# Performance work log

Measured on AMD Instinct MI355X. Metric: run time of the kernel, lower is better.

The kernel has to match this reference:

```python
import jax, jax.numpy as jnp
import numpy as np

N_NODES = 100000
N_EDGES = 1600000
IN_FEAT = 128
HID_FEAT = 128
OUT_FEAT = 128


def setup_inputs() -> dict:
    key = jax.random.key(0)
    k1, k2, k3, k4, k5 = jax.random.split(key, 5)
    x = jax.random.normal(k1, (N_NODES, IN_FEAT), dtype=jnp.float32)
    # Xavier-ish scale for weights
    W_in = jax.random.normal(k2, (2, IN_FEAT, HID_FEAT), dtype=jnp.float32) * (1.0 / np.sqrt(IN_FEAT))
    W_out = jax.random.normal(k3, (2, HID_FEAT, OUT_FEAT), dtype=jnp.float32) * (1.0 / np.sqrt(HID_FEAT))
    src = jax.random.randint(k4, (N_EDGES,), 0, N_NODES, dtype=jnp.int32)
    dst = jax.random.randint(k5, (N_EDGES,), 0, N_NODES, dtype=jnp.int32)
    return {"x": x, "W_in": W_in, "W_out": W_out, "src": src, "dst": dst}


def _mean_aggregate(h, src, dst, num_nodes):
    # copy_src('h','m') + fn.mean('m','neigh'): gather src feats, segment-mean by dst.
    msgs = h[src]                                             # [E, D]
    summed = jax.ops.segment_sum(msgs, dst, num_segments=num_nodes)   # [N, D]
    deg = jax.ops.segment_sum(jnp.ones((src.shape[0],), h.dtype), dst,
                              num_segments=num_nodes)         # [N]
    deg = jnp.maximum(deg, 1.0)                               # zero-in-degree -> 0 output
    return summed / deg[:, None]


def reference(x, W_in, W_out, src, dst):
    n = x.shape[0]
    # Layer 0 (i == 0): uses weight_in, ReLU activation (i != K-1)
    neigh = _mean_aggregate(x, src, dst, n)
    h = x @ W_in[0] + neigh @ W_in[1]
    h = jax.nn.relu(h)
    # Layer 1 (i == K-1): uses weight_out, no activation
    neigh = _mean_aggregate(h, src, dst, n)
    h = h @ W_out[0] + neigh @ W_out[1]
    return h
```

## Files before the change

### kernel.cpp

```cpp
#include <hip/hip_runtime.h>

#define NF 128
#define NBSHIFT 8
#define NBMAX 512
#define CHUNK 4096

typedef __attribute__((ext_vector_type(8))) short bf16x8;
typedef __attribute__((ext_vector_type(4))) float f32x4;
typedef __attribute__((ext_vector_type(2))) float f32x2;

__device__ __forceinline__ unsigned short f2bf(float f) {
    unsigned int u = __builtin_bit_cast(unsigned int, f);
    u = (u + 0x7fffu + ((u >> 16) & 1u)) >> 16;
    return (unsigned short)u;
}
__device__ __forceinline__ float bflo(unsigned int u) {
    return __builtin_bit_cast(float, u << 16);
}
__device__ __forceinline__ float bfhi(unsigned int u) {
    return __builtin_bit_cast(float, u & 0xffff0000u);
}
__device__ __forceinline__ unsigned char f2fp8(float v) {
    return (unsigned char)(__builtin_amdgcn_cvt_pk_fp8_f32(v, v, 0, false) & 0xff);
}

#define BH 256
#define BT 256
__global__ __launch_bounds__(256) void k_prep(const int* __restrict__ dst, int E, int NB,
                                              int* __restrict__ gbhist,
                                              const float* __restrict__ x,
                                              unsigned short* __restrict__ xb,
                                              unsigned char* __restrict__ xq,
                                              const float* __restrict__ Win,
                                              const float* __restrict__ Wout,
                                              unsigned short* __restrict__ BtIn,
                                              unsigned short* __restrict__ BtOut) {
    __shared__ int lh[NBMAX];
    const int bb = blockIdx.x;
    const int t = threadIdx.x;
    if (bb < BH) {
        for (int k = t; k < NBMAX; k += 256) lh[k] = 0;
        __syncthreads();
        for (int i = bb * 256 + t; i < E; i += BH * 256)
            atomicAdd(&lh[((unsigned)dst[i]) >> NBSHIFT], 1);
        __syncthreads();
        for (int k = t; k < NB; k += 256)
            if (lh[k]) atomicAdd(&gbhist[k], lh[k]);
    } else if (bb < BH + BT) {
        int b2 = bb - BH;
        const float* W = (b2 < 128) ? Win : Wout;
        unsigned short* Bt = (b2 < 128) ? BtIn : BtOut;
        int idx = (b2 & 127) * 256 + t;
        int c = idx >> 8;
        int k = idx & 255;
        int p = k >> 7, kk = k & 127;
        Bt[idx] = f2bf(W[((size_t)p * NF + kk) * NF + c]);
    } else {
        long long i = (long long)(bb - BH - BT) * 256 + t;
        const float4 a = *reinterpret_cast<const float4*>(x + i * 8);
        const float4 b = *reinterpret_cast<const float4*>(x + i * 8 + 4);
        union { unsigned short s[8]; uint4 u; } o;
        o.s[0] = f2bf(a.x); o.s[1] = f2bf(a.y); o.s[2] = f2bf(a.z); o.s[3] = f2bf(a.w);
        o.s[4] = f2bf(b.x); o.s[5] = f2bf(b.y); o.s[6] = f2bf(b.z); o.s[7] = f2bf(b.w);
        *reinterpret_cast<uint4*>(xb + i * 8) = o.u;
        int lo = __builtin_amdgcn_cvt_pk_fp8_f32(a.x, a.y, 0, false);
        lo = __builtin_amdgcn_cvt_pk_fp8_f32(a.z, a.w, lo, true);
        int hi = __builtin_amdgcn_cvt_pk_fp8_f32(b.x, b.y, 0, false);
        hi = __builtin_amdgcn_cvt_pk_fp8_f32(b.z, b.w, hi, true);
        uint2 oq; oq.x = (unsigned)lo; oq.y = (unsigned)hi;
        *reinterpret_cast<uint2*>(xq + i * 8) = oq;
    }
}


__global__ __launch_bounds__(256) void k_bscan(const int* __restrict__ gbhist,
                                               int* __restrict__ bbase, int* __restrict__ gcursor,
                                               int NB, int E, int* __restrict__ offsets, int n) {
    __shared__ int sA[NBMAX], sB[NBMAX];
    int t = threadIdx.x;
    for (int k = t; k < NBMAX; k += 256) sA[k] = (k < NB) ? gbhist[k] : 0;
    __syncthreads();
    int* pin = sA;
    int* pout = sB;
    for (int off = 1; off < NBMAX; off <<= 1) {
        for (int k = t; k < NBMAX; k += 256) pout[k] = pin[k] + (k >= off ? pin[k - off] : 0);
        __syncthreads();
        int* tmp = pin; pin = pout; pout = tmp;
    }
    for (int k = t; k < NB; k += 256) {
        int excl = pin[k] - gbhist[k];
        bbase[k] = excl;
        gcursor[k] = excl;
    }
    if (t == 0) {
        bbase[NB] = E;
        offsets[n] = E;
    }
}

__global__ __launch_bounds__(256) void k_bucket(const int* __restrict__ src,
                                                const int* __restrict__ dst,
                                                int* __restrict__ gcursor,
                                                unsigned* __restrict__ gpairs, int E) {
    __shared__ int lhist[NBMAX], lbase[NBMAX], lcur[NBMAX], gb[NBMAX];
    __shared__ int sA[NBMAX], sB[NBMAX];
    __shared__ unsigned stage[CHUNK];
    __shared__ unsigned short stage_b[CHUNK];
    const int t = threadIdx.x;
    const int c0 = blockIdx.x * CHUNK;
    const int cc = min(CHUNK, E - c0);

    for (int k = t; k < NBMAX; k += 256) lhist[k] = 0;
    __syncthreads();

    int ls[16], ld[16];
#pragma unroll
    for (int j = 0; j < 16; ++j) {
        int i = t + j * 256;
        ls[j] = 0; ld[j] = 0;
        if (i < cc) {
            ls[j] = src[c0 + i];
            ld[j] = dst[c0 + i];
            atomicAdd(&lhist[((unsigned)ld[j]) >> NBSHIFT], 1);
        }
    }
    __syncthreads();
    for (int k = t; k < NBMAX; k += 256) sA[k] = lhist[k];
    __syncthreads();
    int* pin = sA;
    int* pout = sB;
    for (int off = 1; off < NBMAX; off <<= 1) {
        for (int k = t; k < NBMAX; k += 256) pout[k] = pin[k] + (k >= off ? pin[k - off] : 0);
        __syncthreads();
        int* tmp = pin; pin = pout; pout = tmp;
    }
    for (int k = t; k < NBMAX; k += 256) {
        int excl = pin[k] - lhist[k];
        lbase[k] = excl;
        lcur[k] = excl;
        int cnt = lhist[k];
        if (cnt > 0) gb[k] = atomicAdd(&gcursor[k], cnt);
    }
    __syncthreads();
#pragma unroll
    for (int j = 0; j < 16; ++j) {
        int i = t + j * 256;
        if (i < cc) {
            int b = ((unsigned)ld[j]) >> NBSHIFT;
            int pos = atomicAdd(&lcur[b], 1);
            stage[pos] = (((unsigned)ld[j] & 255u) << 24) | (unsigned)ls[j];
            stage_b[pos] = (unsigned short)b;
        }
    }
    __syncthreads();
    for (int idx = t; idx < cc; idx += 256) {
        unsigned p = stage[idx];
        int b = stage_b[idx];
        gpairs[gb[b] + (idx - lbase[b])] = p;
    }
}

__global__ __launch_bounds__(256) void k_bsort(const unsigned* __restrict__ gpairs,
                                               const int* __restrict__ bbase,
                                               int* __restrict__ offsets,
                                               float* __restrict__ invdeg,
                                               int* __restrict__ esrc, int n) {
    __shared__ int lcnt[256], lcur[256], sA[256], sB[256];
    const int b = blockIdx.x;
    const int t = threadIdx.x;
    const int base = bbase[b];
    const int c = bbase[b + 1] - base;
    const int n0 = b << NBSHIFT;

    lcnt[t] = 0;
    __syncthreads();
    for (int i = t; i < c; i += 256) {
        int node = (int)(gpairs[base + i] >> 24);
        atomicAdd(&lcnt[node], 1);
    }
    __syncthreads();
    sA[t] = lcnt[t];
    __syncthreads();
    int* pin = sA;
    int* pout = sB;
    for (int off = 1; off < 256; off <<= 1) {
        pout[t] = pin[t] + (t >= off ? pin[t - off] : 0);
        __syncthreads();
        int* tmp = pin; pin = pout; pout = tmp;
    }
    int excl = pin[t] - lcnt[t];
    lcur[t] = excl;
    int node_g = n0 + t;
    if (node_g < n) {
        offsets[node_g] = base + excl;
        invdeg[node_g] = 1.0f / (float)max(lcnt[t], 1);
    }
    __syncthreads();
    for (int i = t; i < c; i += 256) {
        unsigned p = gpairs[base + i];
        int node = (int)(p >> 24);
        int pos = atomicAdd(&lcur[node], 1);
        esrc[base + pos] = (int)(p & 0x00ffffffu);
    }
}

__global__ __launch_bounds__(256) void k_agg_fp8(const unsigned char* __restrict__ feat,
                                                 const int* __restrict__ esrc,
                                                 const int* __restrict__ offsets,
                                                 const float* __restrict__ invdeg,
                                                 unsigned short* __restrict__ neigh, int n) {
    int wid0 = (int)(((long long)blockIdx.x * blockDim.x + threadIdx.x) >> 6);
    const int wid = __builtin_amdgcn_readfirstlane(wid0);
    if (wid >= n) return;
    const int lane = threadIdx.x & 63;
    const int g = lane >> 4;
    const int q = lane & 15;
    const unsigned qoff = (unsigned)q * 8u;
    const unsigned char* fb = feat;

    const int beg = offsets[wid];
    const int end = offsets[wid + 1];
    f32x2 c01 = {0.f, 0.f}, c23 = {0.f, 0.f}, c45 = {0.f, 0.f}, c67 = {0.f, 0.f};

    int i = beg;
    for (; i + 16 <= end; i += 16) {
        int e[16];
#pragma unroll
        for (int j = 0; j < 16; ++j) e[j] = esrc[i + j];
#pragma unroll
        for (int u = 0; u < 4; ++u) {
            int es = (g & 2) ? ((g & 1) ? e[u * 4 + 3] : e[u * 4 + 2])
                             : ((g & 1) ? e[u * 4 + 1] : e[u * 4 + 0]);
            uint2 v = *(const uint2*)(fb + (unsigned)es * 128u + qoff);
            c01 += __builtin_amdgcn_cvt_pk_f32_fp8((int)v.x, false);
            c23 += __builtin_amdgcn_cvt_pk_f32_fp8((int)v.x, true);
            c45 += __builtin_amdgcn_cvt_pk_f32_fp8((int)v.y, false);
            c67 += __builtin_amdgcn_cvt_pk_f32_fp8((int)v.y, true);
        }
    }
    for (; i + 4 <= end; i += 4) {
        int e0 = esrc[i + 0], e1 = esrc[i + 1], e2 = esrc[i + 2], e3 = esrc[i + 3];
        int es = (g & 2) ? ((g & 1) ? e3 : e2) : ((g & 1) ? e1 : e0);
        uint2 v = *(const uint2*)(fb + (unsigned)es * 128u + qoff);
        c01 += __builtin_amdgcn_cvt_pk_f32_fp8((int)v.x, false);
        c23 += __builtin_amdgcn_cvt_pk_f32_fp8((int)v.x, true);
        c45 += __builtin_amdgcn_cvt_pk_f32_fp8((int)v.y, false);
        c67 += __builtin_amdgcn_cvt_pk_f32_fp8((int)v.y, true);
    }
    if (i < end) {
        int r = end - i;
        if (g < r) {
            int es = esrc[i + g];
            uint2 v = *(const uint2*)(fb + (unsigned)es * 128u + qoff);
            c01 += __builtin_amdgcn_cvt_pk_f32_fp8((int)v.x, false);
            c23 += __builtin_amdgcn_cvt_pk_f32_fp8((int)v.x, true);
            c45 += __builtin_amdgcn_cvt_pk_f32_fp8((int)v.y, false);
            c67 += __builtin_amdgcn_cvt_pk_f32_fp8((int)v.y, true);
        }
    }
    float a0 = c01.x, a1 = c01.y, a2 = c23.x, a3 = c23.y;
    float a4 = c45.x, a5 = c45.y, a6 = c67.x, a7 = c67.y;
    a0 += __shfl_xor(a0, 16); a1 += __shfl_xor(a1, 16);
    a2 += __shfl_xor(a2, 16); a3 += __shfl_xor(a3, 16);
    a4 += __shfl_xor(a4, 16); a5 += __shfl_xor(a5, 16);
    a6 += __shfl_xor(a6, 16); a7 += __shfl_xor(a7, 16);
    a0 += __shfl_xor(a0, 32); a1 += __shfl_xor(a1, 32);
    a2 += __shfl_xor(a2, 32); a3 += __shfl_xor(a3, 32);
    a4 += __shfl_xor(a4, 32); a5 += __shfl_xor(a5, 32);
    a6 += __shfl_xor(a6, 32); a7 += __shfl_xor(a7, 32);

    const float sc = invdeg[wid];
    a0 *= sc; a1 *= sc; a2 *= sc; a3 *= sc;
    a4 *= sc; a5 *= sc; a6 *= sc; a7 *= sc;
    unsigned p0, p1, p2, p3;
    asm("v_cvt_pk_bf16_f32 %0, %1, %2" : "=v"(p0) : "v"(a0), "v"(a1));
    asm("v_cvt_pk_bf16_f32 %0, %1, %2" : "=v"(p1) : "v"(a2), "v"(a3));
    asm("v_cvt_pk_bf16_f32 %0, %1, %2" : "=v"(p2) : "v"(a4), "v"(a5));
    asm("v_cvt_pk_bf16_f32 %0, %1, %2" : "=v"(p3) : "v"(a6), "v"(a7));
    if (g == 0) {
        uint4 o; o.x = p0; o.y = p1; o.z = p2; o.w = p3;
        *(uint4*)((char*)neigh + (size_t)wid * 256 + (unsigned)q * 16u) = o;
    }
}

__global__ __launch_bounds__(256) void k_agg_bf16(const unsigned short* __restrict__ feat,
                                                  const int* __restrict__ esrc,
                                                  const int* __restrict__ offsets,
                                                  const float* __restrict__ invdeg,
                                                  unsigned short* __restrict__ neigh, int n) {
    int wid0 = (int)(((long long)blockIdx.x * blockDim.x + threadIdx.x) >> 6);
    const int wid = __builtin_amdgcn_readfirstlane(wid0);
    if (wid >= n) return;
    const int lane = threadIdx.x & 63;
    const int g = lane >> 4;
    const int q = lane & 15;
    const unsigned qoff = (unsigned)q * 16u;
    const char* fb = (const char*)feat;
    const int beg = offsets[wid];
    const int end = offsets[wid + 1];
    float a0 = 0.f, a1 = 0.f, a2 = 0.f, a3 = 0.f, a4 = 0.f, a5 = 0.f, a6 = 0.f, a7 = 0.f;
    int i = beg;
    for (; i + 4 <= end; i += 4) {
        int e0 = esrc[i + 0], e1 = esrc[i + 1], e2 = esrc[i + 2], e3 = esrc[i + 3];
        int es = (g & 2) ? ((g & 1) ? e3 : e2) : ((g & 1) ? e1 : e0);
        uint4 v = *(const uint4*)(fb + (unsigned)es * 256u + qoff);
        a0 += bflo(v.x); a1 += bfhi(v.x);
        a2 += bflo(v.y); a3 += bfhi(v.y);
        a4 += bflo(v.z); a5 += bfhi(v.z);
        a6 += bflo(v.w); a7 += bfhi(v.w);
    }
    if (i < end) {
        int r = end - i;
        if (g < r) {
            int es = esrc[i + g];
            uint4 v = *(const uint4*)(fb + (unsigned)es * 256u + qoff);
            a0 += bflo(v.x); a1 += bfhi(v.x);
            a2 += bflo(v.y); a3 += bfhi(v.y);
            a4 += bflo(v.z); a5 += bfhi(v.z);
            a6 += bflo(v.w); a7 += bfhi(v.w);
        }
    }
    a0 += __shfl_xor(a0, 16); a1 += __shfl_xor(a1, 16);
    a2 += __shfl_xor(a2, 16); a3 += __shfl_xor(a3, 16);
    a4 += __shfl_xor(a4, 16); a5 += __shfl_xor(a5, 16);
    a6 += __shfl_xor(a6, 16); a7 += __shfl_xor(a7, 16);
    a0 += __shfl_xor(a0, 32); a1 += __shfl_xor(a1, 32);
    a2 += __shfl_xor(a2, 32); a3 += __shfl_xor(a3, 32);
    a4 += __shfl_xor(a4, 32); a5 += __shfl_xor(a5, 32);
    a6 += __shfl_xor(a6, 32); a7 += __shfl_xor(a7, 32);
    const float sc = invdeg[wid];
    a0 *= sc; a1 *= sc; a2 *= sc; a3 *= sc;
    a4 *= sc; a5 *= sc; a6 *= sc; a7 *= sc;
    unsigned p0, p1, p2, p3;
    asm("v_cvt_pk_bf16_f32 %0, %1, %2" : "=v"(p0) : "v"(a0), "v"(a1));
    asm("v_cvt_pk_bf16_f32 %0, %1, %2" : "=v"(p1) : "v"(a2), "v"(a3));
    asm("v_cvt_pk_bf16_f32 %0, %1, %2" : "=v"(p2) : "v"(a4), "v"(a5));
    asm("v_cvt_pk_bf16_f32 %0, %1, %2" : "=v"(p3) : "v"(a6), "v"(a7));
    if (g == 0) {
        uint4 o; o.x = p0; o.y = p1; o.z = p2; o.w = p3;
        *(uint4*)((char*)neigh + (size_t)wid * 256 + qoff) = o;
    }
}

__global__ __launch_bounds__(256) void k_agg_f32(const float* __restrict__ feat,
                                                 const int* __restrict__ esrc,
                                                 const int* __restrict__ offsets,
                                                 const float* __restrict__ invdeg,
                                                 unsigned short* __restrict__ neigh, int n) {
    int wid0 = (int)(((long long)blockIdx.x * blockDim.x + threadIdx.x) >> 6);
    const int wid = __builtin_amdgcn_readfirstlane(wid0);
    if (wid >= n) return;
    int lane = threadIdx.x & 63;
    int beg = offsets[wid], end = offsets[wid + 1];
    float a0 = 0.f, a1 = 0.f;
    for (int i = beg; i < end; ++i) {
        int s0 = esrc[i];
        float2 v0 = *(const float2*)(feat + (size_t)s0 * NF + lane * 2);
        a0 += v0.x; a1 += v0.y;
    }
    float sc = invdeg[wid];
    unsigned pk;
    float ca = a0 * sc, cb = a1 * sc;
    asm("v_cvt_pk_bf16_f32 %0, %1, %2" : "=v"(pk) : "v"(ca), "v"(cb));
    *(unsigned*)(neigh + (size_t)wid * NF + lane * 2) = pk;
}

template <bool RELU, bool OUTBF16, bool WRITEQ>
__global__ __launch_bounds__(256) void k_gemm_lds(const unsigned short* __restrict__ A1,
                                                  const unsigned short* __restrict__ A2,
                                                  const unsigned short* __restrict__ Bt,
                                                  void* __restrict__ outv,
                                                  unsigned char* __restrict__ outq,
                                                  int nrows) {
    __shared__ __align__(16) unsigned char sm[32768];
    const int tid = threadIdx.x;
    const int w = tid >> 6;
    const int lane = tid & 63;
    const int l15 = lane & 15;
    const int lk = lane >> 4;
    const int col0 = w * 32;
    const int rbase = blockIdx.x * 64;

#pragma unroll
    for (int h = 0; h < 2; ++h) {
        const unsigned short* Ah = h ? A2 : A1;
#pragma unroll
        for (int j = 0; j < 4; ++j) {
            const int r = w * 16 + j * 4 + lk;
            const int garow = min(rbase + r, nrows - 1);
            const int cch = l15 ^ (r & 7);
            const unsigned short* srcp = Ah + (size_t)garow * NF + cch * 8;
            unsigned char* ldst = &sm[h * 16384 + (w * 16 + j * 4) * 256];
            __builtin_amdgcn_global_load_lds(
                (const __attribute__((address_space(1))) void*)srcp,
                (__attribute__((address_space(3))) void*)ldst, 16, 0, 0);
        }
    }

    bf16x8 breg[2][8];
#pragma unroll
    for (int c = 0; c < 2; ++c)
#pragma unroll
        for (int kc = 0; kc < 8; ++kc)
            breg[c][kc] = *(const bf16x8*)(Bt + (size_t)(col0 + c * 16 + l15) * 256 +
                                           kc * 32 + lk * 8);

    f32x4 acc[4][2];
#pragma unroll
    for (int rc = 0; rc < 4; ++rc) {
        acc[rc][0] = (f32x4)0.0f;
        acc[rc][1] = (f32x4)0.0f;
    }

    __syncthreads();

#pragma unroll
    for (int rc = 0; rc < 4; ++rc) {
        const int row = rc * 16 + l15;
#pragma unroll
        for (int kc = 0; kc < 8; ++kc) {
            const int half = kc >> 2;
            const int kk = kc & 3;
            const int chunk = (kk * 4 + lk) ^ (row & 7);
            const bf16x8 a = *(const bf16x8*)&sm[half * 16384 + row * 256 + chunk * 16];
            acc[rc][0] = __builtin_amdgcn_mfma_f32_16x16x32_bf16(a, breg[0][kc],
                                                                 acc[rc][0], 0, 0, 0);
            acc[rc][1] = __builtin_amdgcn_mfma_f32_16x16x32_bf16(a, breg[1][kc],
                                                                 acc[rc][1], 0, 0, 0);
        }
    }

    __syncthreads();

    if (OUTBF16) {
        unsigned short* smb = (unsigned short*)sm;
        unsigned char* smq = sm + 16384;
#pragma unroll
        for (int rc = 0; rc < 4; ++rc)
#pragma unroll
            for (int r = 0; r < 4; ++r) {
                const int row = rc * 16 + lk * 4 + r;
#pragma unroll
                for (int c = 0; c < 2; ++c) {
                    float v = acc[rc][c][r];
                    if (RELU) v = fmaxf(v, 0.f);
                    const int col = col0 + c * 16 + l15;
                    smb[row * NF + col] = f2bf(v);
                    if (WRITEQ) smq[row * NF + col] = f2fp8(v);
                }
            }
        __syncthreads();
#pragma unroll
        for (int it = 0; it < 4; ++it) {
            const int off = (tid + it * 256) * 16;
            if (rbase + (off >> 8) < nrows)
                *(uint4*)((char*)outv + (size_t)rbase * 256 + off) =
                    *(const uint4*)&sm[off];
        }
        if (WRITEQ) {
#pragma unroll
            for (int it = 0; it < 2; ++it) {
                const int off = (tid + it * 256) * 16;
                if (rbase + (off >> 7) < nrows)
                    *(uint4*)(outq + (size_t)rbase * 128 + off) =
                        *(const uint4*)&sm[16384 + off];
            }
        }
    } else {
        float* smf = (float*)sm;
#pragma unroll
        for (int rc = 0; rc < 4; ++rc)
#pragma unroll
            for (int r = 0; r < 4; ++r) {
                const int row = rc * 16 + lk * 4 + r;
#pragma unroll
                for (int c = 0; c < 2; ++c) {
                    float v = acc[rc][c][r];
                    if (RELU) v = fmaxf(v, 0.f);
                    smf[row * NF + col0 + c * 16 + l15] = v;
                }
            }
        __syncthreads();
#pragma unroll
        for (int it = 0; it < 8; ++it) {
            const int off = (tid + it * 256) * 16;
            if (rbase + (off >> 9) < nrows)
                *(uint4*)((char*)outv + (size_t)rbase * 512 + off) =
                    *(const uint4*)&sm[off];
        }
    }
}

template <bool RELU, bool A1BF16, bool OUTBF16>
__global__ __launch_bounds__(256) void k_gemm_mfma(const void* __restrict__ A1v,
                                                   const unsigned short* __restrict__ A2,
                                                   const unsigned short* __restrict__ Bt,
                                                   void* __restrict__ outv, int nrows) {
    const int tid = threadIdx.x;
    const int wave = tid >> 6;
    const int lane = tid & 63;
    const int l15 = lane & 15;
    const int lk = lane >> 4;
    const int col0 = wave * 32;
    const int rbase = blockIdx.x * 64;

    bf16x8 breg[2][8];
#pragma unroll
    for (int c = 0; c < 2; ++c)
#pragma unroll
        for (int kc = 0; kc < 8; ++kc)
            breg[c][kc] = *(const bf16x8*)(Bt + (size_t)(col0 + c * 16 + l15) * 256 +
                                           kc * 32 + lk * 8);

    f32x4 acc[4][2];
#pragma unroll
    for (int rc = 0; rc < 4; ++rc) {
        acc[rc][0] = (f32x4)0.0f;
        acc[rc][1] = (f32x4)0.0f;
    }

#pragma unroll
    for (int rc = 0; rc < 4; ++rc) {
        const int arow = rbase + rc * 16 + l15;
        const bool ok = arow < nrows;
        bf16x8 a[8];
        if (ok) {
            if (A1BF16) {
                const unsigned short* A1 = (const unsigned short*)A1v;
#pragma unroll
                for (int kc = 0; kc < 4; ++kc) {
                    a[kc] = *(const bf16x8*)(A1 + (size_t)arow * NF + kc * 32 + lk * 8);
                    a[kc + 4] = *(const bf16x8*)(A2 + (size_t)arow * NF + kc * 32 + lk * 8);
                }
            } else {
                const float* A1 = (const float*)A1v;
#pragma unroll
                for (int kc = 0; kc < 4; ++kc) {
                    const float* p = A1 + (size_t)arow * NF + kc * 32 + lk * 8;
                    float4 u = *(const float4*)p;
                    float4 v = *(const float4*)(p + 4);
                    a[kc][0] = (short)f2bf(u.x); a[kc][1] = (short)f2bf(u.y);
                    a[kc][2] = (short)f2bf(u.z); a[kc][3] = (short)f2bf(u.w);
                    a[kc][4] = (short)f2bf(v.x); a[kc][5] = (short)f2bf(v.y);
                    a[kc][6] = (short)f2bf(v.z); a[kc][7] = (short)f2bf(v.w);
                    a[kc + 4] = *(const bf16x8*)(A2 + (size_t)arow * NF + kc * 32 + lk * 8);
                }
            }
        } else {
#pragma unroll
            for (int kc = 0; kc < 8; ++kc) a[kc] = (bf16x8)(short)0;
        }
#pragma unroll
        for (int kc = 0; kc < 8; ++kc) {
            acc[rc][0] = __builtin_amdgcn_mfma_f32_16x16x32_bf16(a[kc], breg[0][kc],
                                                                 acc[rc][0], 0, 0, 0);
            acc[rc][1] = __builtin_amdgcn_mfma_f32_16x16x32_bf16(a[kc], breg[1][kc],
                                                                 acc[rc][1], 0, 0, 0);
        }
    }

#pragma unroll
    for (int rc = 0; rc < 4; ++rc) {
#pragma unroll
        for (int r = 0; r < 4; ++r) {
            const int orow = rbase + rc * 16 + lk * 4 + r;
            if (orow >= nrows) continue;
#pragma unroll
            for (int c = 0; c < 2; ++c) {
                float v = acc[rc][c][r];
                if (RELU) v = fmaxf(v, 0.f);
                const int col = col0 + c * 16 + l15;
                if (OUTBF16)
                    ((unsigned short*)outv)[(size_t)orow * NF + col] = f2bf(v);
                else
                    ((float*)outv)[(size_t)orow * NF + col] = v;
            }
        }
    }
}

extern "C" void kernel_launch(void* const* d_in, const int* in_sizes, int n_in,
                              void* d_out, int out_size, void* d_ws, size_t ws_size,
                              hipStream_t stream) {
    const float* x = (const float*)d_in[0];
    const float* W_in = (const float*)d_in[1];
    const float* W_out = (const float*)d_in[2];
    const int* src = (const int*)d_in[3];
    const int* dst = (const int*)d_in[4];

    const int n = in_sizes[0] / NF;
    const int E = in_sizes[3];
    float* outp = (float*)d_out;

    const int NB = (n + 255) >> NBSHIFT;
    const int nchunks = (E + CHUNK - 1) / CHUNK;

    char* ws = (char*)d_ws;
    size_t off = 0;
    auto take = [&](size_t bytes) {
        void* p = ws + off;
        off = (off + bytes + 511) & ~(size_t)511;
        return p;
    };
    int* gbhist = (int*)take((size_t)NB * 4);
    int* bbase = (int*)take((size_t)(NB + 1) * 4);
    int* gcursor = (int*)take((size_t)NB * 4);
    int* offsets = (int*)take((size_t)(n + 1) * 4);
    float* invdeg = (float*)take((size_t)n * 4);
    unsigned short* BtIn = (unsigned short*)take(128 * 256 * 2);
    unsigned short* BtOut = (unsigned short*)take(128 * 256 * 2);
    unsigned* gpairs = (unsigned*)take((size_t)E * 4);
    int* esrc = (int*)take((size_t)E * 4);
    unsigned short* hb = (unsigned short*)take((size_t)n * NF * 2);
    unsigned short* neigh = (unsigned short*)take((size_t)n * NF * 2);
    size_t need_fp8 = off + (size_t)n * NF * 2 + 512 + (size_t)n * NF + 512 +
                      (size_t)n * NF + 512;
    bool use_fp8 = (ws_size >= need_fp8);
    unsigned short* xb = nullptr;
    unsigned char* xq = nullptr;
    unsigned char* hq = nullptr;
    if (use_fp8) {
        xb = (unsigned short*)take((size_t)n * NF * 2);
        xq = (unsigned char*)take((size_t)n * NF);
        hq = (unsigned char*)take((size_t)n * NF);
    }
    bool use_xb = use_fp8 || (ws_size >= off + (size_t)n * NF * 2);
    if (!use_fp8 && use_xb) xb = (unsigned short*)take((size_t)n * NF * 2);

    hipMemsetAsync(gbhist, 0, (size_t)NB * 4, stream);
    const int cvtBlocks = use_fp8 ? (int)(((long long)n * NF / 8 + 255) / 256) : 0;
    k_prep<<<BH + BT + cvtBlocks, 256, 0, stream>>>(dst, E, NB, gbhist, x, xb, xq,
                                                    W_in, W_out, BtIn, BtOut);
    k_bscan<<<1, 256, 0, stream>>>(gbhist, bbase, gcursor, NB, E, offsets, n);
    k_bucket<<<nchunks, 256, 0, stream>>>(src, dst, gcursor, gpairs, E);
    k_bsort<<<NB, 256, 0, stream>>>(gpairs, bbase, offsets, invdeg, esrc, n);

    const int aggBlocks = (n + 3) / 4;
    const int gemmBlocks = (n + 63) / 64;

    if (use_fp8) {
        k_agg_fp8<<<aggBlocks, 256, 0, stream>>>(xq, esrc, offsets, invdeg, neigh, n);
        k_gemm_lds<true, true, true>
            <<<gemmBlocks, 256, 0, stream>>>(xb, neigh, BtIn, hb, hq, n);
        k_agg_fp8<<<aggBlocks, 256, 0, stream>>>(hq, esrc, offsets, invdeg, neigh, n);
        k_gemm_lds<false, false, false>
            <<<gemmBlocks, 256, 0, stream>>>(hb, neigh, BtOut, outp, nullptr, n);
    } else {
        k_agg_f32<<<aggBlocks, 256, 0, stream>>>(x, esrc, offsets, invdeg, neigh, n);
        k_gemm_mfma<true, false, true>
            <<<gemmBlocks, 256, 0, stream>>>(x, neigh, BtIn, hb, n);
        k_agg_bf16<<<aggBlocks, 256, 0, stream>>>(hb, esrc, offsets, invdeg, neigh, n);
        k_gemm_mfma<false, true, false>
            <<<gemmBlocks, 256, 0, stream>>>(hb, neigh, BtOut, outp, n);
    }
}
```

Before: 198.3 us.

## Sort nodes by degree and aggregate four nodes per wavefront in fp8 path

Adds a degree histogram, a scan and a fill pass that order nodes by in-degree. The fp8 aggregation now gives each 16-lane group its own node, so one wavefront handles four similar-degree nodes. Before, a whole wavefront handled one node and ended with a cross-group shuffle reduction. This removes that reduction and the idle lanes on low-degree tails, and it balances work through degree bucketing. In exchange it adds three small kernels and scattered output writes indexed by node.

Measured after the change: 712.2 us. +259.2%, slower.

```diff
diff --git a/kernel.cpp b/kernel.cpp
--- a/kernel.cpp
+++ b/kernel.cpp
@@ -164,6 +164,8 @@
                                                const int* __restrict__ bbase,
                                                int* __restrict__ offsets,
                                                float* __restrict__ invdeg,
+                                               unsigned char* __restrict__ degb,
+                                               int* __restrict__ gdhist,
                                                int* __restrict__ esrc, int n) {
     __shared__ int lcnt[256], lcur[256], sA[256], sB[256];
     const int b = blockIdx.x;
@@ -194,6 +196,9 @@
     if (node_g < n) {
         offsets[node_g] = base + excl;
         invdeg[node_g] = 1.0f / (float)max(lcnt[t], 1);
+        int d = min(lcnt[t], 255);
+        degb[node_g] = (unsigned char)d;
+        atomicAdd(&gdhist[d], 1);
     }
     __syncthreads();
     for (int i = t; i < c; i += 256) {
@@ -204,82 +209,112 @@
     }
 }
 
-__global__ __launch_bounds__(256) void k_agg_fp8(const unsigned char* __restrict__ feat,
-                                                 const int* __restrict__ esrc,
-                                                 const int* __restrict__ offsets,
-                                                 const float* __restrict__ invdeg,
-                                                 unsigned short* __restrict__ neigh, int n) {
-    int wid0 = (int)(((long long)blockIdx.x * blockDim.x + threadIdx.x) >> 6);
-    const int wid = __builtin_amdgcn_readfirstlane(wid0);
-    if (wid >= n) return;
-    const int lane = threadIdx.x & 63;
+__global__ void k_dscan(const int* __restrict__ gdhist, int* __restrict__ dcur) {
+    __shared__ int sh[256];
+    int t = threadIdx.x;
+    int v = gdhist[t];
+    sh[t] = v;
+    __syncthreads();
+    for (int off = 1; off < 256; off <<= 1) {
+        int x = (t >= off) ? sh[t - off] : 0;
+        __syncthreads();
+        sh[t] += x;
+        __syncthreads();
+    }
+    dcur[t] = sh[t] - v;
+}
+
+__global__ void k_dfill(const unsigned char* __restrict__ degb, int* __restrict__ dcur,
+                        int* __restrict__ dorder, int n) {
+    int i = blockIdx.x * blockDim.x + threadIdx.x;
+    int stride = gridDim.x * blockDim.x;
+    for (; i < n; i += stride) {
+        int d = degb[i];
+        int pos = atomicAdd(&dcur[d], 1);
+        dorder[pos] = i;
+    }
+}
+
+__global__ __launch_bounds__(256) void k_agg4(const unsigned char* __restrict__ feat,
+                                              const int* __restrict__ esrc,
+                                              const int* __restrict__ offsets,
+                                              const float* __restrict__ invdeg,
+                                              const int* __restrict__ dorder,
+                                              unsigned short* __restrict__ neigh, int n) {
+    const int tid = threadIdx.x;
+    const int wv = (int)(((long long)blockIdx.x * blockDim.x + tid) >> 6);
+    if (wv * 4 >= n) return;
+    const int lane = tid & 63;
     const int g = lane >> 4;
     const int q = lane & 15;
+    const int i4 = wv * 4 + g;
+
+    int node = 0, beg = 0, deg = 0;
+    if (i4 < n) {
+        node = dorder[i4];
+        beg = offsets[node];
+        deg = offsets[node + 1] - beg;
+    }
+    int mn = deg, mx = deg;
+    int s1 = __shfl_xor(mn, 16); mn = min(mn, s1);
+    int s2 = __shfl_xor(mx, 16); mx = max(mx, s2);
+    s1 = __shfl_xor(mn, 32); mn = min(mn, s1);
+    s2 = __shfl_xor(mx, 32); mx = max(mx, s2);
+    const int mindeg = __builtin_amdgcn_readfirstlane(mn);
+    const int maxdeg = __builtin_amdgcn_readfirstlane(mx);
+
     const unsigned qoff = (unsigned)q * 8u;
-    const unsigned char* fb = feat;
-
-    const int beg = offsets[wid];
-    const int end = offsets[wid + 1];
     f32x2 c01 = {0.f, 0.f}, c23 = {0.f, 0.f}, c45 = {0.f, 0.f}, c67 = {0.f, 0.f};
 
-    int i = beg;
-    for (; i + 16 <= end; i += 16) {
-        int e[16];
-#pragma unroll
-        for (int j = 0; j < 16; ++j) e[j] = esrc[i + j];
-#pragma unroll
-        for (int u = 0; u < 4; ++u) {
-            int es = (g & 2) ? ((g & 1) ? e[u * 4 + 3] : e[u * 4 + 2])
-                             : ((g & 1) ? e[u * 4 + 1] : e[u * 4 + 0]);
-            uint2 v = *(const uint2*)(fb + (unsigned)es * 128u + qoff);
+    int i = 0;
+    for (; i + 4 <= mindeg; i += 4) {
+        int e0 = esrc[beg + i + 0];
+        int e1 = esrc[beg + i + 1];
+        int e2 = esrc[beg + i + 2];
+        int e3 = esrc[beg + i + 3];
+        uint2 v0 = *(const uint2*)(feat + (unsigned)e0 * 128u + qoff);
+        uint2 v1 = *(const uint2*)(feat + (unsigned)e1 * 128u + qoff);
+        uint2 v2 = *(const uint2*)(feat + (unsigned)e2 * 128u + qoff);
+        uint2 v3 = *(const uint2*)(feat + (unsigned)e3 * 128u + qoff);
+        c01 += __builtin_amdgcn_cvt_pk_f32_fp8((int)v0.x, false);
+        c23 += __builtin_amdgcn_cvt_pk_f32_fp8((int)v0.x, true);
+        c45 += __builtin_amdgcn_cvt_pk_f32_fp8((int)v0.y, false);
+        c67 += __builtin_amdgcn_cvt_pk_f32_fp8((int)v0.y, true);
+        c01 += __builtin_amdgcn_cvt_pk_f32_fp8((int)v1.x, false);
+        c23 += __builtin_amdgcn_cvt_pk_f32_fp8((int)v1.x, true);
+        c45 += __builtin_amdgcn_cvt_pk_f32_fp8((int)v1.y, false);
+        c67 += __builtin_amdgcn_cvt_pk_f32_fp8((int)v1.y, true);
+        c01 += __builtin_amdgcn_cvt_pk_f32_fp8((int)v2.x, false);
+        c23 += __builtin_amdgcn_cvt_pk_f32_fp8((int)v2.x, true);
+        c45 += __builtin_amdgcn_cvt_pk_f32_fp8((int)v2.y, false);
+        c67 += __builtin_amdgcn_cvt_pk_f32_fp8((int)v2.y, true);
+        c01 += __builtin_amdgcn_cvt_pk_f32_fp8((int)v3.x, false);
+        c23 += __builtin_amdgcn_cvt_pk_f32_fp8((int)v3.x, true);
+        c45 += __builtin_amdgcn_cvt_pk_f32_fp8((int)v3.y, false);
+        c67 += __builtin_amdgcn_cvt_pk_f32_fp8((int)v3.y, true);
+    }
+    for (; i < maxdeg; ++i) {
+        if (i < deg) {
+            int e = esrc[beg + i];
+            uint2 v = *(const uint2*)(feat + (unsigned)e * 128u + qoff);
             c01 += __builtin_amdgcn_cvt_pk_f32_fp8((int)v.x, false);
             c23 += __builtin_amdgcn_cvt_pk_f32_fp8((int)v.x, true);
             c45 += __builtin_amdgcn_cvt_pk_f32_fp8((int)v.y, false);
             c67 += __builtin_amdgcn_cvt_pk_f32_fp8((int)v.y, true);
         }
     }
-    for (; i + 4 <= end; i += 4) {
-        int e0 = esrc[i + 0], e1 = esrc[i + 1], e2 = esrc[i + 2], e3 = esrc[i + 3];
-        int es = (g & 2) ? ((g & 1) ? e3 : e2) : ((g & 1) ? e1 : e0);
-        uint2 v = *(const uint2*)(fb + (unsigned)es * 128u + qoff);
-        c01 += __builtin_amdgcn_cvt_pk_f32_fp8((int)v.x, false);
-        c23 += __builtin_amdgcn_cvt_pk_f32_fp8((int)v.x, true);
-        c45 += __builtin_amdgcn_cvt_pk_f32_fp8((int)v.y, false);
-        c67 += __builtin_amdgcn_cvt_pk_f32_fp8((int)v.y, true);
-    }
-    if (i < end) {
-        int r = end - i;
-        if (g < r) {
-            int es = esrc[i + g];
-            uint2 v = *(const uint2*)(fb + (unsigned)es * 128u + qoff);
-            c01 += __builtin_amdgcn_cvt_pk_f32_fp8((int)v.x, false);
-            c23 += __builtin_amdgcn_cvt_pk_f32_fp8((int)v.x, true);
-            c45 += __builtin_amdgcn_cvt_pk_f32_fp8((int)v.y, false);
-            c67 += __builtin_amdgcn_cvt_pk_f32_fp8((int)v.y, true);
-        }
-    }
-    float a0 = c01.x, a1 = c01.y, a2 = c23.x, a3 = c23.y;
-    float a4 = c45.x, a5 = c45.y, a6 = c67.x, a7 = c67.y;
-    a0 += __shfl_xor(a0, 16); a1 += __shfl_xor(a1, 16);
-    a2 += __shfl_xor(a2, 16); a3 += __shfl_xor(a3, 16);
-    a4 += __shfl_xor(a4, 16); a5 += __shfl_xor(a5, 16);
-    a6 += __shfl_xor(a6, 16); a7 += __shfl_xor(a7, 16);
-    a0 += __shfl_xor(a0, 32); a1 += __shfl_xor(a1, 32);
-    a2 += __shfl_xor(a2, 32); a3 += __shfl_xor(a3, 32);
-    a4 += __shfl_xor(a4, 32); a5 += __shfl_xor(a5, 32);
-    a6 += __shfl_xor(a6, 32); a7 += __shfl_xor(a7, 32);
-
-    const float sc = invdeg[wid];
-    a0 *= sc; a1 *= sc; a2 *= sc; a3 *= sc;
-    a4 *= sc; a5 *= sc; a6 *= sc; a7 *= sc;
-    unsigned p0, p1, p2, p3;
-    asm("v_cvt_pk_bf16_f32 %0, %1, %2" : "=v"(p0) : "v"(a0), "v"(a1));
-    asm("v_cvt_pk_bf16_f32 %0, %1, %2" : "=v"(p1) : "v"(a2), "v"(a3));
-    asm("v_cvt_pk_bf16_f32 %0, %1, %2" : "=v"(p2) : "v"(a4), "v"(a5));
-    asm("v_cvt_pk_bf16_f32 %0, %1, %2" : "=v"(p3) : "v"(a6), "v"(a7));
-    if (g == 0) {
+
+    if (i4 < n) {
+        const float sc = invdeg[node];
+        float a0 = c01.x * sc, a1 = c01.y * sc, a2 = c23.x * sc, a3 = c23.y * sc;
+        float a4 = c45.x * sc, a5 = c45.y * sc, a6 = c67.x * sc, a7 = c67.y * sc;
+        unsigned p0, p1, p2, p3;
+        asm("v_cvt_pk_bf16_f32 %0, %1, %2" : "=v"(p0) : "v"(a0), "v"(a1));
+        asm("v_cvt_pk_bf16_f32 %0, %1, %2" : "=v"(p1) : "v"(a2), "v"(a3));
+        asm("v_cvt_pk_bf16_f32 %0, %1, %2" : "=v"(p2) : "v"(a4), "v"(a5));
+        asm("v_cvt_pk_bf16_f32 %0, %1, %2" : "=v"(p3) : "v"(a6), "v"(a7));
         uint4 o; o.x = p0; o.y = p1; o.z = p2; o.w = p3;
-        *(uint4*)((char*)neigh + (size_t)wid * 256 + (unsigned)q * 16u) = o;
+        *(uint4*)((char*)neigh + (size_t)node * 256 + (unsigned)q * 16u) = o;
     }
 }
 
@@ -613,6 +648,10 @@
     int* esrc = (int*)take((size_t)E * 4);
     unsigned short* hb = (unsigned short*)take((size_t)n * NF * 2);
     unsigned short* neigh = (unsigned short*)take((size_t)n * NF * 2);
+    unsigned char* degb = (unsigned char*)take((size_t)n);
+    int* gdhist = (int*)take(256 * 4);
+    int* dcur = (int*)take(256 * 4);
+    int* dorder = (int*)take((size_t)n * 4);
     size_t need_fp8 = off + (size_t)n * NF * 2 + 512 + (size_t)n * NF + 512 +
                       (size_t)n * NF + 512;
     bool use_fp8 = (ws_size >= need_fp8);
@@ -628,24 +667,29 @@
     if (!use_fp8 && use_xb) xb = (unsigned short*)take((size_t)n * NF * 2);
 
     hipMemsetAsync(gbhist, 0, (size_t)NB * 4, stream);
+    hipMemsetAsync(gdhist, 0, 256 * 4, stream);
     const int cvtBlocks = use_fp8 ? (int)(((long long)n * NF / 8 + 255) / 256) : 0;
     k_prep<<<BH + BT + cvtBlocks, 256, 0, stream>>>(dst, E, NB, gbhist, x, xb, xq,
                                                     W_in, W_out, BtIn, BtOut);
     k_bscan<<<1, 256, 0, stream>>>(gbhist, bbase, gcursor, NB, E, offsets, n);
     k_bucket<<<nchunks, 256, 0, stream>>>(src, dst, gcursor, gpairs, E);
-    k_bsort<<<NB, 256, 0, stream>>>(gpairs, bbase, offsets, invdeg, esrc, n);
-
-    const int aggBlocks = (n + 3) / 4;
+    k_bsort<<<NB, 256, 0, stream>>>(gpairs, bbase, offsets, invdeg, degb, gdhist, esrc, n);
+
     const int gemmBlocks = (n + 63) / 64;
 
     if (use_fp8) {
-        k_agg_fp8<<<aggBlocks, 256, 0, stream>>>(xq, esrc, offsets, invdeg, neigh, n);
+        k_dscan<<<1, 256, 0, stream>>>(gdhist, dcur);
+        k_dfill<<<128, 256, 0, stream>>>(degb, dcur, dorder, n);
+
+        const int agg4Blocks = (n + 15) / 16;
+        k_agg4<<<agg4Blocks, 256, 0, stream>>>(xq, esrc, offsets, invdeg, dorder, neigh, n);
         k_gemm_lds<true, true, true>
             <<<gemmBlocks, 256, 0, stream>>>(xb, neigh, BtIn, hb, hq, n);
-        k_agg_fp8<<<aggBlocks, 256, 0, stream>>>(hq, esrc, offsets, invdeg, neigh, n);
+        k_agg4<<<agg4Blocks, 256, 0, stream>>>(hq, esrc, offsets, invdeg, dorder, neigh, n);
         k_gemm_lds<false, false, false>
             <<<gemmBlocks, 256, 0, stream>>>(hb, neigh, BtOut, outp, nullptr, n);
     } else {
+        const int aggBlocks = (n + 3) / 4;
         k_agg_f32<<<aggBlocks, 256, 0, stream>>>(x, esrc, offsets, invdeg, neigh, n);
         k_gemm_mfma<true, false, true>
             <<<gemmBlocks, 256, 0, stream>>>(x, neigh, BtIn, hb, n);
```
